# Performance work log

Measured on AMD Instinct MI355X. Metric: run time of the kernel, lower is better.

## Reference

```python
import jax, jax.numpy as jnp
jax.config.update("jax_enable_x64", True)  # morton codes need int64 bit tricks
import numpy as np

B = 8
N_POINTS = 131072
PATCH = 32
STRIDE = 16
RES = 1024
D_MODEL = 256
L = (N_POINTS - PATCH) // STRIDE + 1  # 8191


def setup_inputs() -> dict:
    key = jax.random.key(0)
    ks = jax.random.split(key, 11)
    def lin_w(k, fin, fout):
        return (jax.random.normal(k, (fin, fout), jnp.float32) / np.sqrt(fin)).astype(jnp.float32)
    return {
        "points": jax.random.normal(ks[0], (B, N_POINTS, 3), jnp.float32),
        # LocalGeometryEncoder mlp: 3 -> 64 -> 128 (ReLU after both)
        "W1": lin_w(ks[1], 3, 64), "b1": jnp.zeros((64,), jnp.float32),
        "W2": lin_w(ks[2], 64, 128), "b2": jnp.zeros((128,), jnp.float32),
        # PositionalEncoding mlp: 3 -> 64 -> 128 (ReLU only after first)
        "Wp1": lin_w(ks[3], 3, 64), "bp1": jnp.zeros((64,), jnp.float32),
        "Wp2": lin_w(ks[4], 64, 128), "bp2": jnp.zeros((128,), jnp.float32),
        # projection: 256 -> d_model
        "Wproj": lin_w(ks[5], 256, D_MODEL), "bproj": jnp.zeros((D_MODEL,), jnp.float32),
    }


def _expand_bits(v):
    v = v.astype(jnp.int64)
    v = (v | (v << 32)) & jnp.int64(8725724278095871)
    v = (v | (v << 16)) & jnp.int64(8725728556220671)
    v = (v | (v << 8)) & jnp.int64(1157144660301377551)
    v = (v | (v << 4)) & jnp.int64(1207822528635744451)
    v = (v | (v << 2)) & jnp.int64(1317624576693539401)
    return v


def _morton_code(points):
    p_min = points.min(axis=1, keepdims=True)
    p_max = points.max(axis=1, keepdims=True)
    scale = jnp.clip(p_max - p_min, 1e-8, None)
    normed = (points - p_min) / scale
    q = jnp.clip((normed * (RES - 1)).astype(jnp.int64), 0, RES - 1)  # [B,N,3]
    return _expand_bits(q[..., 0]) * 4 + _expand_bits(q[..., 1]) * 2 + _expand_bits(q[..., 2])


def reference(points, W1, b1, W2, b2, Wp1, bp1, Wp2, bp2, Wproj, bproj):
    # z-order sort
    morton = _morton_code(points)                 # [B,N] int64
    sort_idx = jnp.argsort(morton, axis=1)        # [B,N]
    sp = jnp.take_along_axis(points, sort_idx[..., None], axis=1)  # [B,N,3]
    # sliding-window unfold -> [B,L,P,3]
    win = jnp.arange(L)[:, None] * STRIDE + jnp.arange(PATCH)[None, :]  # [L,P]
    patches = sp[:, win, :]
    # local geometry encoder
    centroids = patches.mean(axis=2)              # [B,L,3]
    local = patches - centroids[:, :, None, :]    # [B,L,P,3]
    h = jax.nn.relu(jnp.einsum('blpc,cd->blpd', local, W1) + b1)
    feat = jax.nn.relu(jnp.einsum('blpd,de->blpe', h, W2) + b2)  # [B,L,P,128]
    geo = feat.max(axis=2)                        # [B,L,128]
    # positional encoding of centroids
    pos = jax.nn.relu(centroids @ Wp1 + bp1) @ Wp2 + bp2  # [B,L,128]
    combined = jnp.concatenate([geo, pos], axis=-1)       # [B,L,256]
    tokens = combined @ Wproj + bproj                     # [B,L,d_model]
    return tokens, centroids, sort_idx
```

## Files before the change

kernel.cpp:

```cpp
#include <hip/hip_runtime.h>
#include <hip/hip_bf16.h>
#include <stdint.h>

#define B_SZ   8
#define N_PTS  131072
#define L_TOK  8191
#define M_TOK  (B_SZ * L_TOK)

typedef unsigned long long u64;
typedef unsigned int u32;
typedef unsigned short u16;
typedef __hip_bfloat16 bf16;
typedef float f32x4 __attribute__((ext_vector_type(4)));
typedef short bf16x8 __attribute__((ext_vector_type(8)));
typedef u32 u32x4 __attribute__((ext_vector_type(4)));

__device__ __forceinline__ u16 f2bf(float f) {
  u32 u = __float_as_uint(f);
  u32 r = u + 0x7FFFu + ((u >> 16) & 1u);
  return (u16)(r >> 16);
}
__device__ __forceinline__ float bf2f(u16 s) {
  return __uint_as_float(((u32)s) << 16);
}

__device__ __forceinline__ void split_pair(float h0, float h1, u32& hp, u32& lp) {
  asm("v_cvt_pk_bf16_f32 %0, %1, %2" : "=v"(hp) : "v"(h0), "v"(h1));
  float r0 = __uint_as_float(hp << 16);
  float r1 = __uint_as_float(hp & 0xFFFF0000u);
  asm("v_cvt_pk_bf16_f32 %0, %1, %2" : "=v"(lp) : "v"(h0 - r0), "v"(h1 - r1));
}
__device__ __forceinline__ bf16x8 asbf(u32x4 x) {
  union { u32x4 a; bf16x8 b; } u; u.a = x; return u.b;
}

__device__ __forceinline__ u32 f2u_mono(float f) {
  u32 u = __float_as_uint(f);
  return (u & 0x80000000u) ? ~u : (u | 0x80000000u);
}
__device__ __forceinline__ float u2f_mono(u32 u) {
  u32 b = (u & 0x80000000u) ? (u ^ 0x80000000u) : ~u;
  return __uint_as_float(b);
}

__global__ __launch_bounds__(256) void minmax_kernel(const float* __restrict__ pts,
                                                     u32* __restrict__ mm) {
  int b = blockIdx.x >> 6;
  int chunk = blockIdx.x & 63;
  int base = b * N_PTS + chunk * 2048;
  float mn0 = 3.4e38f, mn1 = 3.4e38f, mn2 = 3.4e38f;
  float mx0 = -3.4e38f, mx1 = -3.4e38f, mx2 = -3.4e38f;
  for (int i = threadIdx.x; i < 2048; i += 256) {
    const float* p = pts + (size_t)(base + i) * 3;
    float x = p[0], y = p[1], z = p[2];
    mn0 = fminf(mn0, x); mx0 = fmaxf(mx0, x);
    mn1 = fminf(mn1, y); mx1 = fmaxf(mx1, y);
    mn2 = fminf(mn2, z); mx2 = fmaxf(mx2, z);
  }
  __shared__ u32 smn[3], smx[3];
  if (threadIdx.x < 3) { smn[threadIdx.x] = 0xFFFFFFFFu; smx[threadIdx.x] = 0u; }
  __syncthreads();
  atomicMin(&smn[0], f2u_mono(mn0)); atomicMin(&smn[1], f2u_mono(mn1)); atomicMin(&smn[2], f2u_mono(mn2));
  atomicMax(&smx[0], f2u_mono(mx0)); atomicMax(&smx[1], f2u_mono(mx1)); atomicMax(&smx[2], f2u_mono(mx2));
  __syncthreads();
  if (threadIdx.x < 3)       atomicMin(&mm[b * 3 + threadIdx.x], smn[threadIdx.x]);
  else if (threadIdx.x < 6)  atomicMax(&mm[24 + b * 3 + threadIdx.x - 3], smx[threadIdx.x - 3]);
}

__device__ __forceinline__ u64 expand_bits(u64 v) {
  v = (v | (v << 32)) & 0x001F00000000FFFFull;
  v = (v | (v << 16)) & 0x001F0000FF0000FFull;
  v = (v | (v << 8))  & 0x100F00F00F00F00Full;
  v = (v | (v << 4))  & 0x10C30C30C30C30C3ull;
  v = (v | (v << 2))  & 0x1249249249249249ull;
  return v;
}

__device__ __forceinline__ long long quant1(float p, float mn, float mx) {
  float scale = fmaxf(mx - mn, 1e-8f);
  float num = p - mn;
  float rcp = 1.0f / scale;
  asm volatile("" : "+v"(rcp));
  float normed = num * rcp;
  asm volatile("" : "+v"(normed));
  float scaled = normed * 1023.0f;
  asm volatile("" : "+v"(scaled));
  long long q = (long long)scaled;
  q = q < 0 ? 0 : q; q = q > 1023 ? 1023 : q;
  return q;
}

__global__ __launch_bounds__(256) void morton_kernel(const float* __restrict__ pts,
                                                     const u32* __restrict__ mm,
                                                     u64* __restrict__ keys) {
  int gid = blockIdx.x * 256 + threadIdx.x;
  int b = gid >> 17;
  int i = gid & (N_PTS - 1);
  float mn0 = u2f_mono(mm[b * 3]), mn1 = u2f_mono(mm[b * 3 + 1]), mn2 = u2f_mono(mm[b * 3 + 2]);
  float mx0 = u2f_mono(mm[24 + b * 3]), mx1 = u2f_mono(mm[24 + b * 3 + 1]), mx2 = u2f_mono(mm[24 + b * 3 + 2]);
  const float* p = pts + (size_t)gid * 3;
  long long q0 = quant1(p[0], mn0, mx0);
  long long q1 = quant1(p[1], mn1, mx1);
  long long q2 = quant1(p[2], mn2, mx2);
  u64 m = expand_bits((u64)q0) * 4ull + expand_bits((u64)q1) * 2ull + expand_bits((u64)q2);
  keys[gid] = (m << 17) | (u64)i;
}

__global__ __launch_bounds__(512) void radix_hist(const u64* __restrict__ keys,
                                                  u32* __restrict__ hist,
                                                  u32* __restrict__ tot, int shift) {
  int blk = blockIdx.x;
  int b = blk >> 6, c = blk & 63;
  int t = threadIdx.x;
  __shared__ u32 h[256];
  if (t < 256) h[t] = 0;
  __syncthreads();
  size_t base = ((size_t)b << 17) + (size_t)c * 2048;
  #pragma unroll
  for (int i = 0; i < 4; ++i) {
    u32 d = (u32)((keys[base + i * 512 + t] >> shift) & 255u);
    atomicAdd(&h[d], 1u);
  }
  __syncthreads();
  if (t < 256) {
    u32 v = h[t];
    hist[(blk << 8) + t] = v;
    if (v) atomicAdd(&tot[(b << 8) + t], v);
  }
}

__global__ __launch_bounds__(256) void radix_scan_a(u32* __restrict__ hist) {
  int blk = blockIdx.x;
  int b = blk >> 3, dg = blk & 7;
  int t = threadIdx.x;
  __shared__ u32 H[32 * 65];
  __shared__ u32 part[32 * 8];
  for (int i = t; i < 2048; i += 256) {
    int c = i >> 5, d5 = i & 31;
    H[d5 * 65 + c] = hist[((b * 64 + c) << 8) + dg * 32 + d5];
  }
  __syncthreads();
  int d5 = t & 31, sub = t >> 5;
  u32 s = 0;
  for (int c = sub * 8; c < sub * 8 + 8; ++c) s += H[d5 * 65 + c];
  part[d5 * 8 + sub] = s;
  __syncthreads();
  u32 run = 0;
  for (int k = 0; k < sub; ++k) run += part[d5 * 8 + k];
  for (int c = sub * 8; c < sub * 8 + 8; ++c) {
    u32 x = H[d5 * 65 + c];
    H[d5 * 65 + c] = run;
    run += x;
  }
  __syncthreads();
  for (int i = t; i < 2048; i += 256) {
    int c = i >> 5, d5b = i & 31;
    hist[((b * 64 + c) << 8) + dg * 32 + d5b] = H[d5b * 65 + c];
  }
}

__global__ __launch_bounds__(512) void radix_scatter(const u64* __restrict__ keys_in,
                                                     u64* __restrict__ keys_out,
                                                     const u32* __restrict__ hist,
                                                     const u32* __restrict__ tot,
                                                     int shift) {
  int blk = blockIdx.x;
  int b = blk >> 6, c = blk & 63;
  int t = threadIdx.x;
  int w = t >> 6, lane = t & 63;
  __shared__ u32 whist[8][256];
  __shared__ u32 gbase[256];
  __shared__ u32 sd[256];
  for (int i = t; i < 2048; i += 512) ((u32*)whist)[i] = 0u;
  u32 my = 0;
  if (t < 256) {
    my = tot[(b << 8) + t];
    sd[t] = my;
    gbase[t] = hist[(blk << 8) + t];
  }
  __syncthreads();
  #pragma unroll
  for (int off = 1; off < 256; off <<= 1) {
    u32 v = (t >= off && t < 256) ? sd[t - off] : 0u;
    __syncthreads();
    if (t < 256) sd[t] += v;
    __syncthreads();
  }
  if (t < 256) gbase[t] += sd[t] - my;
  size_t base = ((size_t)b << 17) + (size_t)c * 2048;
  u64 key[4]; u32 dig[4]; u32 loff[4];
  #pragma unroll
  for (int i = 0; i < 4; ++i) {
    key[i] = keys_in[base + w * 256 + i * 64 + lane];
    dig[i] = (u32)((key[i] >> shift) & 255u);
  }
  #pragma unroll
  for (int i = 0; i < 4; ++i) {
    u64 m = ~0ull;
    #pragma unroll
    for (int k = 0; k < 8; ++k) {
      u64 bb = __ballot((dig[i] >> k) & 1u);
      m &= ((dig[i] >> k) & 1u) ? bb : ~bb;
    }
    u32 rank = (u32)__popcll(m & ((1ull << lane) - 1ull));
    u32 cnt = (u32)__popcll(m);
    int leader = (int)__ffsll((unsigned long long)m) - 1;
    u32 prev = 0;
    if (lane == leader) prev = atomicAdd(&whist[w][dig[i]], cnt);
    prev = __shfl(prev, leader);
    loff[i] = prev + rank;
  }
  __syncthreads();
  if (t < 256) {
    u32 run = 0;
    #pragma unroll
    for (int ww = 0; ww < 8; ++ww) { u32 v = whist[ww][t]; whist[ww][t] = run; run += v; }
  }
  __syncthreads();
  #pragma unroll
  for (int i = 0; i < 4; ++i) {
    u32 dst = gbase[dig[i]] + whist[w][dig[i]] + loff[i];
    keys_out[((size_t)b << 17) + dst] = key[i];
  }
}

__global__ __launch_bounds__(512) void scatter_final(
    const u64* __restrict__ keys_in, const u32* __restrict__ hist,
    const u32* __restrict__ tot,
    const float* __restrict__ pts, float* __restrict__ sp, float* __restrict__ sidx,
    const float* __restrict__ Wproj, const float* __restrict__ W2,
    const float* __restrict__ Wp2,
    u16* __restrict__ wfrag, u16* __restrict__ w2f, u16* __restrict__ wp2f) {
  int bid = blockIdx.x;
  int t = threadIdx.x;
  if (bid >= 512) {
    int fb = bid - 512;
    if (fb < 128) {
      int e = fb * 512 + t;
      int k = e >> 8, n = e & 255;
      float v = Wproj[e];
      u16 hb = f2bf(v);
      u16 lb = f2bf(v - bf2f(hb));
      int ks = k >> 5, q = (k >> 3) & 3, j = k & 7;
      int nt = n >> 4, ln2 = n & 15;
      int base = ((ks * 16 + nt) * 64 + q * 16 + ln2) * 8 + j;
      wfrag[base] = hb;
      wfrag[65536 + base] = lb;
    } else {
      const float* W = (fb < 144) ? W2 : Wp2;
      u16* frag = (fb < 144) ? w2f : wp2f;
      int e = ((fb < 144) ? (fb - 128) : (fb - 144)) * 512 + t;
      int k = e >> 7, n = e & 127;
      float v = W[e];
      u16 hb = f2bf(v);
      u16 lb = f2bf(v - bf2f(hb));
      int kc = k >> 5, q = (k >> 3) & 3, j = k & 7;
      int nt = n >> 4, ln2 = n & 15;
      int base = ((kc * 8 + nt) * 64 + q * 16 + ln2) * 8 + j;
      frag[base] = hb;
      frag[8192 + base] = lb;
    }
    return;
  }
  int blk = bid;
  int b = blk >> 6, c = blk & 63;
  int w = t >> 6, lane = t & 63;
  __shared__ u32 whist[8][256];
  __shared__ u32 gbase[256];
  __shared__ u32 sd[256];
  for (int i = t; i < 2048; i += 512) ((u32*)whist)[i] = 0u;
  u32 my = 0;
  if (t < 256) {
    my = tot[(b << 8) + t];
    sd[t] = my;
    gbase[t] = hist[(blk << 8) + t];
  }
  __syncthreads();
  #pragma unroll
  for (int off = 1; off < 256; off <<= 1) {
    u32 v = (t >= off && t < 256) ? sd[t - off] : 0u;
    __syncthreads();
    if (t < 256) sd[t] += v;
    __syncthreads();
  }
  if (t < 256) gbase[t] += sd[t] - my;
  size_t base = ((size_t)b << 17) + (size_t)c * 2048;
  u64 key[4]; u32 dig[4]; u32 loff[4];
  #pragma unroll
  for (int i = 0; i < 4; ++i) {
    key[i] = keys_in[base + w * 256 + i * 64 + lane];
    dig[i] = (u32)((key[i] >> 41) & 255u);
  }
  #pragma unroll
  for (int i = 0; i < 4; ++i) {
    u64 m = ~0ull;
    #pragma unroll
    for (int k = 0; k < 8; ++k) {
      u64 bb = __ballot((dig[i] >> k) & 1u);
      m &= ((dig[i] >> k) & 1u) ? bb : ~bb;
    }
    u32 rank = (u32)__popcll(m & ((1ull << lane) - 1ull));
    u32 cnt = (u32)__popcll(m);
    int leader = (int)__ffsll((unsigned long long)m) - 1;
    u32 prev = 0;
    if (lane == leader) prev = atomicAdd(&whist[w][dig[i]], cnt);
    prev = __shfl(prev, leader);
    loff[i] = prev + rank;
  }
  __syncthreads();
  if (t < 256) {
    u32 run = 0;
    #pragma unroll
    for (int ww = 0; ww < 8; ++ww) { u32 v = whist[ww][t]; whist[ww][t] = run; run += v; }
  }
  __syncthreads();
  #pragma unroll
  for (int i = 0; i < 4; ++i) {
    u32 dst = gbase[dig[i]] + whist[w][dig[i]] + loff[i];
    int idx = (int)(key[i] & 0x1FFFFull);
    u32 gid = ((u32)b << 17) + dst;
    sidx[gid] = (float)idx;
    const float* s = pts + ((size_t)(b << 17) + idx) * 3;
    float* dp = sp + (size_t)gid * 3;
    dp[0] = s[0]; dp[1] = s[1]; dp[2] = s[2];
  }
}

__global__ __launch_bounds__(512) void patch_kernel(
    const float* __restrict__ sp,
    const float* __restrict__ W1, const float* __restrict__ b1,
    const u16* __restrict__ W2g, const float* __restrict__ b2,
    const float* __restrict__ Wp1, const float* __restrict__ bp1,
    const u16* __restrict__ Wp2g, const float* __restrict__ bp2,
    bf16* __restrict__ comb, float* __restrict__ cent_out) {
  __shared__ float ptsS[6192];
  __shared__ float cenS[384];
  __shared__ float w1p[256];
  __shared__ float wpp[256];
  __shared__ float b2s[128];
  __shared__ float bp2s[128];
  __shared__ __align__(16) u16 W2frag[16384];

  int t = threadIdx.x;
  int bib = blockIdx.x;
  int b = blockIdx.y;
  int l0 = bib * 128;
  int pcount = min(128, L_TOK - l0);

  {
    const float4* src4 = (const float4*)(sp + (size_t)b * (N_PTS * 3) + (size_t)l0 * 48);
    int nvec = min(1548, ((N_PTS - l0 * 16) * 3) >> 2);
    float4* dst4 = (float4*)ptsS;
    for (int i = t; i < nvec; i += 512) dst4[i] = src4[i];
  }
  {
    const float4* s4 = (const float4*)W2g;
    float4* d4 = (float4*)W2frag;
    for (int i = t; i < 2048; i += 512) d4[i] = s4[i];
  }
  if (t < 64) {
    w1p[t] = W1[t]; w1p[64 + t] = W1[64 + t];
    w1p[128 + t] = W1[128 + t]; w1p[192 + t] = b1[t];
  } else if (t < 128) {
    int i = t - 64;
    wpp[i] = Wp1[i]; wpp[64 + i] = Wp1[64 + i];
    wpp[128 + i] = Wp1[128 + i]; wpp[192 + i] = bp1[i];
  } else if (t < 256) {
    b2s[t - 128] = b2[t - 128];
  } else if (t < 384) {
    bp2s[t - 256] = bp2[t - 256];
  }
  __syncthreads();

  if (t < 384) {
    int pa = t / 3, c = t - pa * 3;
    if (pa < pcount) {
      float s = 0.f;
      for (int i = 0; i < 32; ++i) {
        int ii = (i + pa) & 31;
        s += ptsS[(pa * 16 + ii) * 3 + c];
      }
      float cv = s * (1.0f / 32.0f);
      cenS[pa * 3 + c] = cv;
      cent_out[(size_t)(b * L_TOK + l0 + pa) * 3 + c] = cv;
    }
  }
  __syncthreads();

  int w = t >> 6, lane = t & 63, ln = lane & 15, quad = lane >> 4;
  const bf16x8* Bf = (const bf16x8*)W2frag;

  for (int ig = 0; ig < 16; ++ig) {
    int ll = w * 16 + ig;
    if (ll >= pcount) break;
    float cx = cenS[ll * 3], cy = cenS[ll * 3 + 1], cz = cenS[ll * 3 + 2];
    float xs[2], ys[2], zs[2];
    #pragma unroll
    for (int mt = 0; mt < 2; ++mt) {
      int row = ll * 16 + mt * 16 + ln;
      xs[mt] = ptsS[row * 3] - cx;
      ys[mt] = ptsS[row * 3 + 1] - cy;
      zs[mt] = ptsS[row * 3 + 2] - cz;
    }
    u32x4 Ahi[2][2], Alo[2][2];
    #pragma unroll
    for (int kc = 0; kc < 2; ++kc)
      #pragma unroll
      for (int w4 = 0; w4 < 4; ++w4) {
        int col = kc * 32 + quad * 8 + w4 * 2;
        float wx0 = w1p[col],     wy0 = w1p[64 + col],     wz0 = w1p[128 + col],     wb0 = w1p[192 + col];
        float wx1 = w1p[col + 1], wy1 = w1p[64 + col + 1], wz1 = w1p[128 + col + 1], wb1 = w1p[192 + col + 1];
        #pragma unroll
        for (int mt = 0; mt < 2; ++mt) {
          float h0 = fmaxf(fmaf(xs[mt], wx0, fmaf(ys[mt], wy0, fmaf(zs[mt], wz0, wb0))), 0.f);
          float h1 = fmaxf(fmaf(xs[mt], wx1, fmaf(ys[mt], wy1, fmaf(zs[mt], wz1, wb1))), 0.f);
          u32 hp, lp;
          split_pair(h0, h1, hp, lp);
          Ahi[mt][kc][w4] = hp;
          Alo[mt][kc][w4] = lp;
        }
      }
    bf16x8 Ah[2][2], Al[2][2];
    #pragma unroll
    for (int mt = 0; mt < 2; ++mt)
      #pragma unroll
      for (int kc = 0; kc < 2; ++kc) { Ah[mt][kc] = asbf(Ahi[mt][kc]); Al[mt][kc] = asbf(Alo[mt][kc]); }

    size_t tokoff = (size_t)(b * L_TOK + l0 + ll) * 256;
    #pragma unroll
    for (int half = 0; half < 2; ++half) {
      f32x4 acc[2][4];
      #pragma unroll
      for (int mt = 0; mt < 2; ++mt)
        #pragma unroll
        for (int n4 = 0; n4 < 4; ++n4) acc[mt][n4] = (f32x4){0.f, 0.f, 0.f, 0.f};
      #pragma unroll
      for (int n4 = 0; n4 < 4; ++n4) {
        int nt = half * 4 + n4;
        bf16x8 Bh0 = Bf[(0 * 8 + nt) * 64 + lane];
        bf16x8 Bh1 = Bf[(1 * 8 + nt) * 64 + lane];
        bf16x8 Bl0 = Bf[1024 + (0 * 8 + nt) * 64 + lane];
        bf16x8 Bl1 = Bf[1024 + (1 * 8 + nt) * 64 + lane];
        #pragma unroll
        for (int mt = 0; mt < 2; ++mt) {
          acc[mt][n4] = __builtin_amdgcn_mfma_f32_16x16x32_bf16(Ah[mt][0], Bh0, acc[mt][n4], 0, 0, 0);
          acc[mt][n4] = __builtin_amdgcn_mfma_f32_16x16x32_bf16(Ah[mt][1], Bh1, acc[mt][n4], 0, 0, 0);
          acc[mt][n4] = __builtin_amdgcn_mfma_f32_16x16x32_bf16(Al[mt][0], Bh0, acc[mt][n4], 0, 0, 0);
          acc[mt][n4] = __builtin_amdgcn_mfma_f32_16x16x32_bf16(Al[mt][1], Bh1, acc[mt][n4], 0, 0, 0);
          acc[mt][n4] = __builtin_amdgcn_mfma_f32_16x16x32_bf16(Ah[mt][0], Bl0, acc[mt][n4], 0, 0, 0);
          acc[mt][n4] = __builtin_amdgcn_mfma_f32_16x16x32_bf16(Ah[mt][1], Bl1, acc[mt][n4], 0, 0, 0);
        }
      }
      #pragma unroll
      for (int n4 = 0; n4 < 4; ++n4) {
        int col = (half * 4 + n4) * 16 + ln;
        float bv = b2s[col];
        float m = 0.f;
        #pragma unroll
        for (int mt = 0; mt < 2; ++mt)
          #pragma unroll
          for (int r = 0; r < 4; ++r) m = fmaxf(m, acc[mt][n4][r] + bv);
        m = fmaxf(m, __shfl_xor(m, 16));
        m = fmaxf(m, __shfl_xor(m, 32));
        if (lane < 16) comb[tokoff + col] = __float2bfloat16(m);
      }
    }
  }

  {
    int lrow = w * 16 + ln;
    int lcl = min(lrow, pcount - 1);
    float cx = cenS[lcl * 3], cy = cenS[lcl * 3 + 1], cz = cenS[lcl * 3 + 2];
    u32x4 Ahi[2], Alo[2];
    #pragma unroll
    for (int kc = 0; kc < 2; ++kc)
      #pragma unroll
      for (int w4 = 0; w4 < 4; ++w4) {
        int col = kc * 32 + quad * 8 + w4 * 2;
        float h0 = fmaxf(fmaf(cx, wpp[col], fmaf(cy, wpp[64 + col], fmaf(cz, wpp[128 + col], wpp[192 + col]))), 0.f);
        float h1 = fmaxf(fmaf(cx, wpp[col + 1], fmaf(cy, wpp[64 + col + 1], fmaf(cz, wpp[128 + col + 1], wpp[192 + col + 1]))), 0.f);
        u32 hp, lp;
        split_pair(h0, h1, hp, lp);
        Ahi[kc][w4] = hp;
        Alo[kc][w4] = lp;
      }
    bf16x8 A0h = asbf(Ahi[0]), A1h = asbf(Ahi[1]), A0l = asbf(Alo[0]), A1l = asbf(Alo[1]);
    const bf16x8* Pf = (const bf16x8*)Wp2g;
    f32x4 acc[8];
    #pragma unroll
    for (int nt = 0; nt < 8; ++nt) acc[nt] = (f32x4){0.f, 0.f, 0.f, 0.f};
    #pragma unroll
    for (int nt = 0; nt < 8; ++nt) {
      bf16x8 Bh0 = Pf[(0 * 8 + nt) * 64 + lane];
      bf16x8 Bh1 = Pf[(8 + nt) * 64 + lane];
      bf16x8 Bl0 = Pf[1024 + (0 * 8 + nt) * 64 + lane];
      bf16x8 Bl1 = Pf[1024 + (8 + nt) * 64 + lane];
      acc[nt] = __builtin_amdgcn_mfma_f32_16x16x32_bf16(A0h, Bh0, acc[nt], 0, 0, 0);
      acc[nt] = __builtin_amdgcn_mfma_f32_16x16x32_bf16(A1h, Bh1, acc[nt], 0, 0, 0);
      acc[nt] = __builtin_amdgcn_mfma_f32_16x16x32_bf16(A0l, Bh0, acc[nt], 0, 0, 0);
      acc[nt] = __builtin_amdgcn_mfma_f32_16x16x32_bf16(A1l, Bh1, acc[nt], 0, 0, 0);
      acc[nt] = __builtin_amdgcn_mfma_f32_16x16x32_bf16(A0h, Bl0, acc[nt], 0, 0, 0);
      acc[nt] = __builtin_amdgcn_mfma_f32_16x16x32_bf16(A1h, Bl1, acc[nt], 0, 0, 0);
    }
    #pragma unroll
    for (int nt = 0; nt < 8; ++nt)
      #pragma unroll
      for (int r = 0; r < 4; ++r) {
        int lr = w * 16 + quad * 4 + r;
        if (lr < pcount) {
          float v = acc[nt][r] + bp2s[nt * 16 + ln];
          comb[(size_t)(b * L_TOK + l0 + lr) * 256 + 128 + nt * 16 + ln] = __float2bfloat16(v);
        }
      }
  }
}

__global__ __launch_bounds__(256) void proj_mfma(const bf16* __restrict__ A,
                                                 const u16* __restrict__ fragG,
                                                 const float* __restrict__ bias,
                                                 float* __restrict__ C) {
  int t = threadIdx.x;
  int w = t >> 6, lane = t & 63, ln = lane & 15, quad = lane >> 4;
  int mg = blockIdx.x >> 1;
  int nh = blockIdx.x & 1;
  int tile0 = mg * 16 + w * 4;
  const bf16x8* Bf = (const bf16x8*)fragG;

  bf16x8 Af[4][8];
  const bf16x8 zero8 = (bf16x8){0, 0, 0, 0, 0, 0, 0, 0};
  #pragma unroll
  for (int mt = 0; mt < 4; ++mt) {
    int row = (tile0 + mt) * 16 + ln;
    bool ok = row < M_TOK;
    const bf16x8* ap = (const bf16x8*)(A + (size_t)(ok ? row : 0) * 256);
    #pragma unroll
    for (int ks = 0; ks < 8; ++ks) {
      bf16x8 v = ap[ks * 4 + quad];
      Af[mt][ks] = ok ? v : zero8;
    }
  }

  for (int nt2 = 0; nt2 < 8; ++nt2) {
    int nt = nh * 8 + nt2;
    f32x4 acc[4];
    #pragma unroll
    for (int mt = 0; mt < 4; ++mt) acc[mt] = (f32x4){0.f, 0.f, 0.f, 0.f};
    #pragma unroll
    for (int ks = 0; ks < 8; ++ks) {
      bf16x8 Bh = Bf[(ks * 16 + nt) * 64 + lane];
      bf16x8 Bl = Bf[8192 + (ks * 16 + nt) * 64 + lane];
      #pragma unroll
      for (int mt = 0; mt < 4; ++mt)
        acc[mt] = __builtin_amdgcn_mfma_f32_16x16x32_bf16(Af[mt][ks], Bh, acc[mt], 0, 0, 0);
      #pragma unroll
      for (int mt = 0; mt < 4; ++mt)
        acc[mt] = __builtin_amdgcn_mfma_f32_16x16x32_bf16(Af[mt][ks], Bl, acc[mt], 0, 0, 0);
    }
    int col = nt * 16 + ln;
    float bv = bias[col];
    #pragma unroll
    for (int mt = 0; mt < 4; ++mt)
      #pragma unroll
      for (int r = 0; r < 4; ++r) {
        int row = (tile0 + mt) * 16 + quad * 4 + r;
        if (row < M_TOK) C[(size_t)row * 256 + col] = acc[mt][r] + bv;
      }
  }
}

extern "C" void kernel_launch(void* const* d_in, const int* in_sizes, int n_in,
                              void* d_out, int out_size, void* d_ws, size_t ws_size,
                              hipStream_t stream) {
  const float* points = (const float*)d_in[0];
  const float* W1 = (const float*)d_in[1];
  const float* b1 = (const float*)d_in[2];
  const float* W2 = (const float*)d_in[3];
  const float* b2 = (const float*)d_in[4];
  const float* Wp1 = (const float*)d_in[5];
  const float* bp1 = (const float*)d_in[6];
  const float* Wp2 = (const float*)d_in[7];
  const float* bp2 = (const float*)d_in[8];
  const float* Wproj = (const float*)d_in[9];
  const float* bproj = (const float*)d_in[10];

  float* out = (float*)d_out;
  float* tokens = out;
  float* cents  = out + 16775168;
  float* sidx   = out + 16971752;

  char* ws = (char*)d_ws;
  u32* mm     = (u32*)ws;
  u64* keysA  = (u64*)(ws + 256);
  float* sp   = (float*)(ws + 256 + 8388608);
  char* combB = ws + 256 + 8388608 + 12582912;
  bf16* comb  = (bf16*)combB;
  u64* keysB  = (u64*)combB;
  u32* hist   = (u32*)(combB + 8388608);
  u32* totG   = (u32*)(combB + 8388608 + 2097152);
  u16* wfrag  = (u16*)(ws + 256);
  u16* w2fg   = (u16*)(ws + 256 + 262144);
  u16* wp2fg  = (u16*)(ws + 256 + 262144 + 32768);

  hipMemsetAsync(mm, 0xFF, 96, stream);
  hipMemsetAsync((char*)mm + 96, 0x00, 96, stream);
  hipMemsetAsync(totG, 0x00, 4 * 2048 * 4, stream);
  minmax_kernel<<<512, 256, 0, stream>>>(points, mm);
  morton_kernel<<<4096, 256, 0, stream>>>(points, mm, keysA);

  const int shifts[4] = {17, 25, 33, 41};
  u64* src = keysA; u64* dst = keysB;
  for (int p = 0; p < 3; ++p) {
    radix_hist<<<512, 512, 0, stream>>>(src, hist, totG + p * 2048, shifts[p]);
    radix_scan_a<<<64, 256, 0, stream>>>(hist);
    radix_scatter<<<512, 512, 0, stream>>>(src, dst, hist, totG + p * 2048, shifts[p]);
    u64* tmp = src; src = dst; dst = tmp;
  }
  radix_hist<<<512, 512, 0, stream>>>(src, hist, totG + 3 * 2048, shifts[3]);
  radix_scan_a<<<64, 256, 0, stream>>>(hist);
  scatter_final<<<672, 512, 0, stream>>>(src, hist, totG + 3 * 2048, points, sp, sidx,
                                         Wproj, W2, Wp2, wfrag, w2fg, wp2fg);

  patch_kernel<<<dim3(64, 8), 512, 0, stream>>>(sp, W1, b1, w2fg, b2,
                                                Wp1, bp1, wp2fg, bp2, comb, cents);
  proj_mfma<<<512, 256, 0, stream>>>(comb, wfrag, bproj, tokens);
}
```

Before: 349.5 us.

## Fuse radix digit histograms into morton and previous scatter passes

The separate radix_hist kernels are removed. The first-pass digit histogram is built inside the morton kernel, and each scatter pass builds the next pass's per-chunk histogram and per-batch totals with atomics, using each key's destination chunk. Histogram zeroing moves into the minmax kernel, which replaces the memset, and each pass gets its own histogram slice. The aim is to avoid re-reading all keys and to cut four kernel launches per sort. In exchange it adds about one million global atomics per pass, and these may contend because sorted keys cluster by chunk.

```diff
diff --git a/kernel.cpp b/kernel.cpp
--- a/kernel.cpp
+++ b/kernel.cpp
@@ -44,7 +44,13 @@
 }
 
 __global__ __launch_bounds__(256) void minmax_kernel(const float* __restrict__ pts,
-                                                     u32* __restrict__ mm) {
+                                                     u32* __restrict__ mm,
+                                                     u32* __restrict__ histz,
+                                                     u32* __restrict__ totz) {
+  int gt = blockIdx.x * 256 + threadIdx.x;
+  #pragma unroll
+  for (int k = 0; k < 4; ++k) histz[gt + k * 131072] = 0u;
+  if (gt < 8192) totz[gt] = 0u;
   int b = blockIdx.x >> 6;
   int chunk = blockIdx.x & 63;
   int base = b * N_PTS + chunk * 2048;
@@ -92,8 +98,13 @@
 
 __global__ __launch_bounds__(256) void morton_kernel(const float* __restrict__ pts,
                                                      const u32* __restrict__ mm,
-                                                     u64* __restrict__ keys) {
-  int gid = blockIdx.x * 256 + threadIdx.x;
+                                                     u64* __restrict__ keys,
+                                                     u32* __restrict__ hist0,
+                                                     u32* __restrict__ tot0) {
+  __shared__ u32 h[256];
+  int t = threadIdx.x;
+  h[t] = 0;
+  int gid = blockIdx.x * 256 + t;
   int b = gid >> 17;
   int i = gid & (N_PTS - 1);
   float mn0 = u2f_mono(mm[b * 3]), mn1 = u2f_mono(mm[b * 3 + 1]), mn2 = u2f_mono(mm[b * 3 + 2]);
@@ -104,28 +115,14 @@
   long long q2 = quant1(p[2], mn2, mx2);
   u64 m = expand_bits((u64)q0) * 4ull + expand_bits((u64)q1) * 2ull + expand_bits((u64)q2);
   keys[gid] = (m << 17) | (u64)i;
-}
-
-__global__ __launch_bounds__(512) void radix_hist(const u64* __restrict__ keys,
-                                                  u32* __restrict__ hist,
-                                                  u32* __restrict__ tot, int shift) {
-  int blk = blockIdx.x;
-  int b = blk >> 6, c = blk & 63;
-  int t = threadIdx.x;
-  __shared__ u32 h[256];
-  if (t < 256) h[t] = 0;
-  __syncthreads();
-  size_t base = ((size_t)b << 17) + (size_t)c * 2048;
-  #pragma unroll
-  for (int i = 0; i < 4; ++i) {
-    u32 d = (u32)((keys[base + i * 512 + t] >> shift) & 255u);
-    atomicAdd(&h[d], 1u);
-  }
-  __syncthreads();
-  if (t < 256) {
-    u32 v = h[t];
-    hist[(blk << 8) + t] = v;
-    if (v) atomicAdd(&tot[(b << 8) + t], v);
+  __syncthreads();
+  atomicAdd(&h[(u32)(m & 255ull)], 1u);
+  __syncthreads();
+  u32 v = h[t];
+  if (v) {
+    int c = (blockIdx.x & 511) >> 3;
+    atomicAdd(&hist0[((b * 64 + c) << 8) + t], v);
+    atomicAdd(&tot0[(b << 8) + t], v);
   }
 }
 
@@ -163,7 +160,9 @@
                                                      u64* __restrict__ keys_out,
                                                      const u32* __restrict__ hist,
                                                      const u32* __restrict__ tot,
-                                                     int shift) {
+                                                     u32* __restrict__ histN,
+                                                     u32* __restrict__ totN,
+                                                     int shift, int shiftN) {
   int blk = blockIdx.x;
   int b = blk >> 6, c = blk & 63;
   int t = threadIdx.x;
@@ -171,9 +170,11 @@
   __shared__ u32 whist[8][256];
   __shared__ u32 gbase[256];
   __shared__ u32 sd[256];
+  __shared__ u32 h2[256];
   for (int i = t; i < 2048; i += 512) ((u32*)whist)[i] = 0u;
   u32 my = 0;
   if (t < 256) {
+    h2[t] = 0u;
     my = tot[(b << 8) + t];
     sd[t] = my;
     gbase[t] = hist[(blk << 8) + t];
@@ -221,7 +222,13 @@
   for (int i = 0; i < 4; ++i) {
     u32 dst = gbase[dig[i]] + whist[w][dig[i]] + loff[i];
     keys_out[((size_t)b << 17) + dst] = key[i];
-  }
+    u32 dn = (u32)((key[i] >> shiftN) & 255u);
+    int cn = (int)(dst >> 11);
+    atomicAdd(&histN[((b * 64 + cn) << 8) + dn], 1u);
+    atomicAdd(&h2[dn], 1u);
+  }
+  __syncthreads();
+  if (t < 256 && h2[t]) atomicAdd(&totN[(b << 8) + t], h2[t]);
 }
 
 __global__ __launch_bounds__(512) void scatter_final(
@@ -595,7 +602,7 @@
   char* combB = ws + 256 + 8388608 + 12582912;
   bf16* comb  = (bf16*)combB;
   u64* keysB  = (u64*)combB;
-  u32* hist   = (u32*)(combB + 8388608);
+  u32* histA  = (u32*)(combB + 8388608);
   u32* totG   = (u32*)(combB + 8388608 + 2097152);
   u16* wfrag  = (u16*)(ws + 256);
   u16* w2fg   = (u16*)(ws + 256 + 262144);
@@ -603,21 +610,21 @@
 
   hipMemsetAsync(mm, 0xFF, 96, stream);
   hipMemsetAsync((char*)mm + 96, 0x00, 96, stream);
-  hipMemsetAsync(totG, 0x00, 4 * 2048 * 4, stream);
-  minmax_kernel<<<512, 256, 0, stream>>>(points, mm);
-  morton_kernel<<<4096, 256, 0, stream>>>(points, mm, keysA);
-
-  const int shifts[4] = {17, 25, 33, 41};
-  u64* src = keysA; u64* dst = keysB;
-  for (int p = 0; p < 3; ++p) {
-    radix_hist<<<512, 512, 0, stream>>>(src, hist, totG + p * 2048, shifts[p]);
-    radix_scan_a<<<64, 256, 0, stream>>>(hist);
-    radix_scatter<<<512, 512, 0, stream>>>(src, dst, hist, totG + p * 2048, shifts[p]);
-    u64* tmp = src; src = dst; dst = tmp;
-  }
-  radix_hist<<<512, 512, 0, stream>>>(src, hist, totG + 3 * 2048, shifts[3]);
-  radix_scan_a<<<64, 256, 0, stream>>>(hist);
-  scatter_final<<<672, 512, 0, stream>>>(src, hist, totG + 3 * 2048, points, sp, sidx,
+  minmax_kernel<<<512, 256, 0, stream>>>(points, mm, histA, totG);
+  morton_kernel<<<4096, 256, 0, stream>>>(points, mm, keysA, histA, totG);
+
+  radix_scan_a<<<64, 256, 0, stream>>>(histA);
+  radix_scatter<<<512, 512, 0, stream>>>(keysA, keysB, histA, totG,
+                                         histA + 131072, totG + 2048, 17, 25);
+  radix_scan_a<<<64, 256, 0, stream>>>(histA + 131072);
+  radix_scatter<<<512, 512, 0, stream>>>(keysB, keysA, histA + 131072, totG + 2048,
+                                         histA + 262144, totG + 4096, 25, 33);
+  radix_scan_a<<<64, 256, 0, stream>>>(histA + 262144);
+  radix_scatter<<<512, 512, 0, stream>>>(keysA, keysB, histA + 262144, totG + 4096,
+                                         histA + 393216, totG + 6144, 33, 41);
+  radix_scan_a<<<64, 256, 0, stream>>>(histA + 393216);
+  scatter_final<<<672, 512, 0, stream>>>(keysB, histA + 393216, totG + 6144,
+                                         points, sp, sidx,
                                          Wproj, W2, Wp2, wfrag, w2fg, wp2fg);
 
   patch_kernel<<<dim3(64, 8), 512, 0, stream>>>(sp, W1, b1, w2fg, b2,
```

After: 456.6 us. 1.31x slower.
